# Optimization experiments

Hardware: AMD Instinct MI355X
Metric: run time of the kernel (lower is better)

Reference implementation:

```python
import jax, jax.numpy as jnp
import numpy as np

MARGIN = 0.2


def colbert_score(q, d):
    # q: (B, Q, D), d: (B, K, D) -> scalar
    sim = jnp.einsum('bqd,bkd->bqk', q, d)          # (B, Q, K)
    max_sim = jnp.max(sim, axis=2)                   # (B, Q) row-wise max over doc tokens
    return jnp.sum(max_sim)                          # sum over query tokens and batch


def setup_inputs() -> dict:
    key = jax.random.key(0)
    k1, k2, k3 = jax.random.split(key, 3)
    B, Q, K, D = 256, 256, 512, 128
    return {
        'q': jax.random.normal(k1, (B, Q, D), dtype=jnp.float32),
        'p': jax.random.normal(k2, (B, K, D), dtype=jnp.float32),
        'n': jax.random.normal(k3, (B, K, D), dtype=jnp.float32),
    }


def reference(q, p, n):
    pos_score = colbert_score(q, p)
    neg_score = colbert_score(q, n)
    loss = jax.nn.relu(MARGIN + neg_score - pos_score)
    # torch .mean() on a scalar is identity
    return loss
```

## Files before the change

kernel.cpp:

```cpp
#include <hip/hip_runtime.h>


#define MARGIN   0.2f
#define Bn       256
#define Qn       256
#define Kn       512
#define Dn       128
#define TN       32
#define NT       (Kn / TN)
#define BSTR     136
#define NTHREADS 256
#define MI       2

typedef __attribute__((ext_vector_type(8))) short short8;
typedef __attribute__((ext_vector_type(4))) short short4v;
typedef __attribute__((ext_vector_type(4))) float f32x4;

__device__ __forceinline__ void split_trunc(float x, unsigned short& hi, unsigned short& lo) {
    unsigned int u = __float_as_uint(x);
    hi = (unsigned short)(u >> 16);
    float l = x - __uint_as_float(u & 0xFFFF0000u);
    lo = (unsigned short)(__float_as_uint(l) >> 16);
}

__global__ __launch_bounds__(NTHREADS, 4)
void colbert_q4_kernel(const float* __restrict__ qg,
                       const float* __restrict__ pg,
                       const float* __restrict__ ng,
                       double* __restrict__ sum_ws) {
    __shared__ short Bs[2][2][TN * BSTR];
    __shared__ float part[4];

    const int tid  = threadIdx.x;
    const int w    = tid >> 6;
    const int lane = tid & 63;
    const int l16  = lane & 15;
    const int quad = lane >> 4;
    const int b    = blockIdx.x;
    const int pass = blockIdx.y;
    const int qh   = blockIdx.z;

    const float* docb = (pass ? ng : pg) + (size_t)b * Kn * Dn;

    float4 pre[4];
    {
        const float4* s4 = (const float4*)docb;
#pragma unroll
        for (int k = 0; k < 4; ++k) pre[k] = s4[tid + 256 * k];
    }

    short8 Ahi[MI][4], Alo[MI][4];
    {
        const float* qb = qg + ((size_t)b * Qn + qh * 128) * Dn;
#pragma unroll
        for (int mi = 0; mi < MI; ++mi)
#pragma unroll
            for (int ks = 0; ks < 4; ++ks) {
                const float* src = qb + (size_t)(w * 32 + mi * 16 + l16) * Dn
                                      + ks * 32 + quad * 8;
                float4 v0 = *(const float4*)src;
                float4 v1 = *(const float4*)(src + 4);
                float x[8] = {v0.x, v0.y, v0.z, v0.w, v1.x, v1.y, v1.z, v1.w};
#pragma unroll
                for (int j = 0; j < 8; ++j) {
                    unsigned short h, l;
                    split_trunc(x[j], h, l);
                    Ahi[mi][ks][j] = (short)h;
                    Alo[mi][ks][j] = (short)l;
                }
            }
    }

    float maxv[MI][4];
#pragma unroll
    for (int mi = 0; mi < MI; ++mi)
#pragma unroll
        for (int r = 0; r < 4; ++r) maxv[mi][r] = -3e38f;

    int buf = 0;
    for (int t = 0; t < NT; ++t) {
#pragma unroll
        for (int k = 0; k < 4; ++k) {
            int i   = tid + 256 * k;
            int doc = i >> 5;
            int d4  = i & 31;
            float4 v = pre[k];
            float x[4] = {v.x, v.y, v.z, v.w};
            short4v hi, lo;
#pragma unroll
            for (int j = 0; j < 4; ++j) {
                unsigned short h, l;
                split_trunc(x[j], h, l);
                hi[j] = (short)h;
                lo[j] = (short)l;
            }
            *(short4v*)&Bs[buf][0][doc * BSTR + d4 * 4] = hi;
            *(short4v*)&Bs[buf][1][doc * BSTR + d4 * 4] = lo;
        }
        __syncthreads();

        if (t + 1 < NT) {
            const float4* s4 = (const float4*)(docb + (size_t)(t + 1) * TN * Dn);
#pragma unroll
            for (int k = 0; k < 4; ++k) pre[k] = s4[tid + 256 * k];
        }

        f32x4 acc[MI][2];
#pragma unroll
        for (int mi = 0; mi < MI; ++mi)
#pragma unroll
            for (int ni = 0; ni < 2; ++ni) acc[mi][ni] = (f32x4){0.f, 0.f, 0.f, 0.f};

#pragma unroll
        for (int ni = 0; ni < 2; ++ni) {
#pragma unroll
            for (int ks = 0; ks < 4; ++ks) {
                int off = (ni * 16 + l16) * BSTR + ks * 32 + quad * 8;
                short8 bhi = *(const short8*)&Bs[buf][0][off];
                short8 blo = *(const short8*)&Bs[buf][1][off];
#pragma unroll
                for (int mi = 0; mi < MI; ++mi)
                    acc[mi][ni] = __builtin_amdgcn_mfma_f32_16x16x32_bf16(
                        Ahi[mi][ks], bhi, acc[mi][ni], 0, 0, 0);
#pragma unroll
                for (int mi = 0; mi < MI; ++mi)
                    acc[mi][ni] = __builtin_amdgcn_mfma_f32_16x16x32_bf16(
                        Alo[mi][ks], bhi, acc[mi][ni], 0, 0, 0);
#pragma unroll
                for (int mi = 0; mi < MI; ++mi)
                    acc[mi][ni] = __builtin_amdgcn_mfma_f32_16x16x32_bf16(
                        Ahi[mi][ks], blo, acc[mi][ni], 0, 0, 0);
            }
        }

#pragma unroll
        for (int mi = 0; mi < MI; ++mi)
#pragma unroll
            for (int r = 0; r < 4; ++r)
                maxv[mi][r] = fmaxf(maxv[mi][r], fmaxf(acc[mi][0][r], acc[mi][1][r]));
        buf ^= 1;
    }

#pragma unroll
    for (int off = 1; off < 16; off <<= 1)
#pragma unroll
        for (int mi = 0; mi < MI; ++mi)
#pragma unroll
            for (int r = 0; r < 4; ++r)
                maxv[mi][r] = fmaxf(maxv[mi][r], __shfl_xor(maxv[mi][r], off));

    float s = 0.f;
#pragma unroll
    for (int mi = 0; mi < MI; ++mi)
#pragma unroll
        for (int r = 0; r < 4; ++r) s += maxv[mi][r];
    if (l16 != 0) s = 0.f;
    s += __shfl_xor(s, 16);
    s += __shfl_xor(s, 32);
    if (lane == 0) part[w] = s;
    __syncthreads();
    if (tid == 0) {
        double t = (double)part[0] + part[1] + part[2] + part[3];
        atomicAdd(sum_ws, pass ? -t : t);
    }
}

__global__ void finalize_kernel(const double* __restrict__ sum_ws,
                                float* __restrict__ out) {
    out[0] = fmaxf(0.0f, MARGIN - (float)sum_ws[0]);
}

extern "C" void kernel_launch(void* const* d_in, const int* in_sizes, int n_in,
                              void* d_out, int out_size, void* d_ws, size_t ws_size,
                              hipStream_t stream) {
    const float* q = (const float*)d_in[0];
    const float* p = (const float*)d_in[1];
    const float* n = (const float*)d_in[2];
    float* out = (float*)d_out;
    double* ws = (double*)d_ws;

    hipMemsetAsync(ws, 0, sizeof(double), stream);

    colbert_q4_kernel<<<dim3(Bn, 2, 2), NTHREADS, 0, stream>>>(q, p, n, ws);
    finalize_kernel<<<1, 1, 0, stream>>>(ws, out);
}
```

Baseline: 183.1 us.

## Interleave bf16 split staging and global prefetch with MFMA loop, one barrier per tile

The doc-tile loop is restructured so that staging the next tile into the other LDS buffer and prefetching the tile after it happen between MFMA groups of the current tile, leaving a single barrier per iteration. The hi/lo bf16 split now uses byte-permute packing instead of per-element shorts. The three product terms go into separate accumulators, which breaks the serial MFMA dependency chain at the cost of extra registers. The aim is to hide global-load and conversion latency behind matrix work and shorten MFMA dependency stalls, with a risk of register pressure under the 4-block launch bound.

```diff
diff --git a/kernel.cpp b/kernel.cpp
--- a/kernel.cpp
+++ b/kernel.cpp
@@ -13,21 +13,53 @@
 #define MI       2
 
 typedef __attribute__((ext_vector_type(8))) short short8;
-typedef __attribute__((ext_vector_type(4))) short short4v;
 typedef __attribute__((ext_vector_type(4))) float f32x4;
 
-__device__ __forceinline__ void split_trunc(float x, unsigned short& hi, unsigned short& lo) {
-    unsigned int u = __float_as_uint(x);
-    hi = (unsigned short)(u >> 16);
-    float l = x - __uint_as_float(u & 0xFFFF0000u);
-    lo = (unsigned short)(__float_as_uint(l) >> 16);
+__device__ __forceinline__ unsigned int pack_hi_bits(unsigned int ua, unsigned int ub) {
+    return __builtin_amdgcn_perm(ub, ua, 0x07060302);
+}
+
+__device__ __forceinline__ void stage_chunk(short* __restrict__ hiP,
+                                            short* __restrict__ loP,
+                                            int doc, int d4, float4 v) {
+    unsigned ux = __float_as_uint(v.x), uy = __float_as_uint(v.y);
+    unsigned uz = __float_as_uint(v.z), uw = __float_as_uint(v.w);
+    float lx = v.x - __uint_as_float(ux & 0xFFFF0000u);
+    float ly = v.y - __uint_as_float(uy & 0xFFFF0000u);
+    float lz = v.z - __uint_as_float(uz & 0xFFFF0000u);
+    float lw = v.w - __uint_as_float(uw & 0xFFFF0000u);
+    uint2 hi, lo;
+    hi.x = pack_hi_bits(ux, uy);
+    hi.y = pack_hi_bits(uz, uw);
+    lo.x = pack_hi_bits(__float_as_uint(lx), __float_as_uint(ly));
+    lo.y = pack_hi_bits(__float_as_uint(lz), __float_as_uint(lw));
+    *(uint2*)&hiP[doc * BSTR + d4 * 4] = hi;
+    *(uint2*)&loP[doc * BSTR + d4 * 4] = lo;
+}
+
+__device__ __forceinline__ void cvt8(const float* __restrict__ src,
+                                     short8& hi, short8& lo) {
+    float4 v0 = *(const float4*)src;
+    float4 v1 = *(const float4*)(src + 4);
+    float x[8] = {v0.x, v0.y, v0.z, v0.w, v1.x, v1.y, v1.z, v1.w};
+    union { unsigned u[4]; short8 s; } H, L;
+#pragma unroll
+    for (int k = 0; k < 4; ++k) {
+        unsigned u0 = __float_as_uint(x[2 * k]);
+        unsigned u1 = __float_as_uint(x[2 * k + 1]);
+        float l0 = x[2 * k]     - __uint_as_float(u0 & 0xFFFF0000u);
+        float l1 = x[2 * k + 1] - __uint_as_float(u1 & 0xFFFF0000u);
+        H.u[k] = pack_hi_bits(u0, u1);
+        L.u[k] = pack_hi_bits(__float_as_uint(l0), __float_as_uint(l1));
+    }
+    hi = H.s; lo = L.s;
 }
 
 __global__ __launch_bounds__(NTHREADS, 4)
-void colbert_q4_kernel(const float* __restrict__ qg,
-                       const float* __restrict__ pg,
-                       const float* __restrict__ ng,
-                       double* __restrict__ sum_ws) {
+void colbert_pipe_kernel(const float* __restrict__ qg,
+                         const float* __restrict__ pg,
+                         const float* __restrict__ ng,
+                         double* __restrict__ sum_ws) {
     __shared__ short Bs[2][2][TN * BSTR];
     __shared__ float part[4];
 
@@ -41,6 +73,7 @@
     const int qh   = blockIdx.z;
 
     const float* docb = (pass ? ng : pg) + (size_t)b * Kn * Dn;
+    const int   d4    = tid & 31;
 
     float4 pre[4];
     {
@@ -55,90 +88,81 @@
 #pragma unroll
         for (int mi = 0; mi < MI; ++mi)
 #pragma unroll
+            for (int ks = 0; ks < 4; ++ks)
+                cvt8(qb + (size_t)(w * 32 + mi * 16 + l16) * Dn + ks * 32 + quad * 8,
+                     Ahi[mi][ks], Alo[mi][ks]);
+    }
+
+    float maxv[MI][4];
+#pragma unroll
+    for (int mi = 0; mi < MI; ++mi)
+#pragma unroll
+        for (int r = 0; r < 4; ++r) maxv[mi][r] = -3e38f;
+
+    {
+#pragma unroll
+        for (int k = 0; k < 4; ++k) {
+            int doc = (tid + 256 * k) >> 5;
+            stage_chunk(&Bs[0][0][0], &Bs[0][1][0], doc, d4, pre[k]);
+        }
+        const float4* s4 = (const float4*)(docb + (size_t)TN * Dn);
+#pragma unroll
+        for (int k = 0; k < 4; ++k) pre[k] = s4[tid + 256 * k];
+    }
+    __syncthreads();
+
+    for (int t = 0; t < NT; ++t) {
+        const int cur = t & 1, nxt = cur ^ 1;
+        const int tload = (t + 2 < NT) ? t + 2 : NT - 1;
+        const float4* s4n = (const float4*)(docb + (size_t)tload * TN * Dn);
+
+#pragma unroll
+        for (int ni = 0; ni < 2; ++ni) {
+            f32x4 a0[MI], a1[MI], a2[MI];
+#pragma unroll
+            for (int mi = 0; mi < MI; ++mi) {
+                a0[mi] = (f32x4){0.f, 0.f, 0.f, 0.f};
+                a1[mi] = (f32x4){0.f, 0.f, 0.f, 0.f};
+                a2[mi] = (f32x4){0.f, 0.f, 0.f, 0.f};
+            }
+#pragma unroll
             for (int ks = 0; ks < 4; ++ks) {
-                const float* src = qb + (size_t)(w * 32 + mi * 16 + l16) * Dn
-                                      + ks * 32 + quad * 8;
-                float4 v0 = *(const float4*)src;
-                float4 v1 = *(const float4*)(src + 4);
-                float x[8] = {v0.x, v0.y, v0.z, v0.w, v1.x, v1.y, v1.z, v1.w};
-#pragma unroll
-                for (int j = 0; j < 8; ++j) {
-                    unsigned short h, l;
-                    split_trunc(x[j], h, l);
-                    Ahi[mi][ks][j] = (short)h;
-                    Alo[mi][ks][j] = (short)l;
+                const int off = (ni * 16 + l16) * BSTR + ks * 32 + quad * 8;
+                short8 bhi = *(const short8*)&Bs[cur][0][off];
+                short8 blo = *(const short8*)&Bs[cur][1][off];
+
+                const int it = ni * 4 + ks;
+                if (it < 4) {
+                    if (t + 1 < NT) {
+                        int doc = (tid + 256 * it) >> 5;
+                        stage_chunk(&Bs[nxt][0][0], &Bs[nxt][1][0], doc, d4, pre[it]);
+                    }
+                } else {
+                    pre[it - 4] = s4n[tid + 256 * (it - 4)];
                 }
+
+#pragma unroll
+                for (int mi = 0; mi < MI; ++mi)
+                    a0[mi] = __builtin_amdgcn_mfma_f32_16x16x32_bf16(
+                        Ahi[mi][ks], bhi, a0[mi], 0, 0, 0);
+#pragma unroll
+                for (int mi = 0; mi < MI; ++mi)
+                    a1[mi] = __builtin_amdgcn_mfma_f32_16x16x32_bf16(
+                        Alo[mi][ks], bhi, a1[mi], 0, 0, 0);
+#pragma unroll
+                for (int mi = 0; mi < MI; ++mi)
+                    a2[mi] = __builtin_amdgcn_mfma_f32_16x16x32_bf16(
+                        Ahi[mi][ks], blo, a2[mi], 0, 0, 0);
             }
-    }
-
-    float maxv[MI][4];
-#pragma unroll
-    for (int mi = 0; mi < MI; ++mi)
-#pragma unroll
-        for (int r = 0; r < 4; ++r) maxv[mi][r] = -3e38f;
-
-    int buf = 0;
-    for (int t = 0; t < NT; ++t) {
-#pragma unroll
-        for (int k = 0; k < 4; ++k) {
-            int i   = tid + 256 * k;
-            int doc = i >> 5;
-            int d4  = i & 31;
-            float4 v = pre[k];
-            float x[4] = {v.x, v.y, v.z, v.w};
-            short4v hi, lo;
-#pragma unroll
-            for (int j = 0; j < 4; ++j) {
-                unsigned short h, l;
-                split_trunc(x[j], h, l);
-                hi[j] = (short)h;
-                lo[j] = (short)l;
-            }
-            *(short4v*)&Bs[buf][0][doc * BSTR + d4 * 4] = hi;
-            *(short4v*)&Bs[buf][1][doc * BSTR + d4 * 4] = lo;
+#pragma unroll
+            for (int mi = 0; mi < MI; ++mi)
+#pragma unroll
+                for (int r = 0; r < 4; ++r) {
+                    float s = a0[mi][r] + a1[mi][r] + a2[mi][r];
+                    maxv[mi][r] = fmaxf(maxv[mi][r], s);
+                }
         }
         __syncthreads();
-
-        if (t + 1 < NT) {
-            const float4* s4 = (const float4*)(docb + (size_t)(t + 1) * TN * Dn);
-#pragma unroll
-            for (int k = 0; k < 4; ++k) pre[k] = s4[tid + 256 * k];
-        }
-
-        f32x4 acc[MI][2];
-#pragma unroll
-        for (int mi = 0; mi < MI; ++mi)
-#pragma unroll
-            for (int ni = 0; ni < 2; ++ni) acc[mi][ni] = (f32x4){0.f, 0.f, 0.f, 0.f};
-
-#pragma unroll
-        for (int ni = 0; ni < 2; ++ni) {
-#pragma unroll
-            for (int ks = 0; ks < 4; ++ks) {
-                int off = (ni * 16 + l16) * BSTR + ks * 32 + quad * 8;
-                short8 bhi = *(const short8*)&Bs[buf][0][off];
-                short8 blo = *(const short8*)&Bs[buf][1][off];
-#pragma unroll
-                for (int mi = 0; mi < MI; ++mi)
-                    acc[mi][ni] = __builtin_amdgcn_mfma_f32_16x16x32_bf16(
-                        Ahi[mi][ks], bhi, acc[mi][ni], 0, 0, 0);
-#pragma unroll
-                for (int mi = 0; mi < MI; ++mi)
-                    acc[mi][ni] = __builtin_amdgcn_mfma_f32_16x16x32_bf16(
-                        Alo[mi][ks], bhi, acc[mi][ni], 0, 0, 0);
-#pragma unroll
-                for (int mi = 0; mi < MI; ++mi)
-                    acc[mi][ni] = __builtin_amdgcn_mfma_f32_16x16x32_bf16(
-                        Ahi[mi][ks], blo, acc[mi][ni], 0, 0, 0);
-            }
-        }
-
-#pragma unroll
-        for (int mi = 0; mi < MI; ++mi)
-#pragma unroll
-            for (int r = 0; r < 4; ++r)
-                maxv[mi][r] = fmaxf(maxv[mi][r], fmaxf(acc[mi][0][r], acc[mi][1][r]));
-        buf ^= 1;
     }
 
 #pragma unroll
@@ -181,6 +205,6 @@
 
     hipMemsetAsync(ws, 0, sizeof(double), stream);
 
-    colbert_q4_kernel<<<dim3(Bn, 2, 2), NTHREADS, 0, stream>>>(q, p, n, ws);
+    colbert_pipe_kernel<<<dim3(Bn, 2, 2), NTHREADS, 0, stream>>>(q, p, n, ws);
     finalize_kernel<<<1, 1, 0, stream>>>(ws, out);
 }
```

Result: slower. 238.9 us (+30.5%).
